# Optimization experiments

Hardware: AMD Instinct MI355X
Metric: run time of the kernel (lower is better)

The kernel has to match this reference:

```python
import jax, jax.numpy as jnp
import numpy as np

D_MODEL = 1024
NUM_HEADS = 16
D_K = D_MODEL // NUM_HEADS  # 64
THETA = 10000.0
B, S = 2, 2048


def _rope(x, cos, sin):
    # x: [b, h, s, d]; cos/sin: [s, d//2] (broadcast over b, h)
    x1 = x[..., 0::2]
    x2 = x[..., 1::2]
    y1 = x1 * cos - x2 * sin
    y2 = x1 * sin + x2 * cos
    # interleave back: stack on last dim then flatten pairs
    return jnp.stack([y1, y2], axis=-1).reshape(x.shape)


def setup_inputs() -> dict:
    key = jax.random.key(0)
    ks = jax.random.split(key, 5)
    scale = 1.0 / np.sqrt(D_MODEL)
    return {
        "x": jax.random.normal(ks[0], (B, S, D_MODEL), dtype=jnp.float32),
        "token_positions": jnp.arange(S, dtype=jnp.int32),
        "Wq": jax.random.normal(ks[1], (D_MODEL, D_MODEL), dtype=jnp.float32) * scale,
        "Wk": jax.random.normal(ks[2], (D_MODEL, D_MODEL), dtype=jnp.float32) * scale,
        "Wv": jax.random.normal(ks[3], (D_MODEL, D_MODEL), dtype=jnp.float32) * scale,
        "Wo": jax.random.normal(ks[4], (D_MODEL, D_MODEL), dtype=jnp.float32) * scale,
    }


def reference(x, token_positions, Wq, Wk, Wv, Wo):
    b, s, _ = x.shape
    # torch nn.Linear semantics (no bias in this repo's Linear): y = x @ W.T
    q = jnp.einsum("bsd,od->bso", x, Wq)
    k = jnp.einsum("bsd,od->bso", x, Wk)
    v = jnp.einsum("bsd,od->bso", x, Wv)
    # split heads: b s (h d) -> b h s d
    def split(t):
        return t.reshape(b, s, NUM_HEADS, D_K).transpose(0, 2, 1, 3)
    q, k, v = split(q), split(k), split(v)

    # RoPE tables
    inv_freq = 1.0 / (THETA ** (jnp.arange(0, D_K, 2, dtype=jnp.float32) / D_K))  # [d/2]
    freqs = token_positions.astype(jnp.float32)[:, None] * inv_freq[None, :]      # [s, d/2]
    cos, sin = jnp.cos(freqs), jnp.sin(freqs)
    q = _rope(q, cos, sin)
    k = _rope(k, cos, sin)

    scale = D_K ** (-0.5)
    scores = jnp.einsum("bhqd,bhkd->bhqk", q, k) * scale  # [b,h,s,s]
    causal = jnp.tril(jnp.ones((s, s), dtype=bool))
    scores = jnp.where(causal, scores, -jnp.inf)
    attn = jax.nn.softmax(scores, axis=-1)
    out = jnp.einsum("bhqk,bhkd->bhqd", attn, v)
    out = out.transpose(0, 2, 1, 3).reshape(b, s, D_MODEL)  # b h s d -> b s (h d)
    return jnp.einsum("bsd,od->bso", out, Wo)
```

## Files before the change

kernel.cpp:

```cpp
#include <hip/hip_runtime.h>
#include <hip/hip_bf16.h>
#include <math.h>

#define SS 2048

typedef __attribute__((ext_vector_type(8))) __bf16 bf16x8;
typedef __attribute__((ext_vector_type(4))) float f32x4;
typedef __attribute__((ext_vector_type(16))) float f32x16;
typedef __attribute__((ext_vector_type(4))) unsigned int u32x4;
typedef __attribute__((ext_vector_type(4))) unsigned short u16x4;

__device__ __forceinline__ f32x4 mfma16(bf16x8 a, bf16x8 b, f32x4 c) {
  return __builtin_amdgcn_mfma_f32_16x16x32_bf16(a, b, c, 0, 0, 0);
}
__device__ __forceinline__ f32x16 mfma32(bf16x8 a, bf16x8 b, f32x16 c) {
  return __builtin_amdgcn_mfma_f32_32x32x16_bf16(a, b, c, 0, 0, 0);
}

__device__ __forceinline__ void gld_lds16(const void* g, void* l) {
  __builtin_amdgcn_global_load_lds(
      (__attribute__((address_space(1))) void*)(g),
      (__attribute__((address_space(3))) void*)(l), 16, 0, 0);
}

#if __has_builtin(__builtin_amdgcn_exp2f)
#define EXP2F(x) __builtin_amdgcn_exp2f(x)
#else
#define EXP2F(x) __expf(0.69314718056f * (x))
#endif

__device__ __forceinline__ unsigned int cvtpk_bf16(float lo, float hi) {
  unsigned int r;
  asm("v_cvt_pk_bf16_f32 %0, %1, %2" : "=v"(r) : "v"(lo), "v"(hi));
  return r;
}
__device__ __forceinline__ void swap32(unsigned int& x, unsigned int& y) {
  asm("v_permlane32_swap_b32 %0, %1" : "+v"(x), "+v"(y));
}
__device__ __forceinline__ unsigned short bfu(float v) {
  __bf16 h = (__bf16)v;
  return __builtin_bit_cast(unsigned short, h);
}

__global__ void prep_kernel(const float* __restrict__ x, const float* __restrict__ Wq,
                            const float* __restrict__ Wk, const float* __restrict__ Wv,
                            const float* __restrict__ Wo, const int* __restrict__ pos,
                            __bf16* __restrict__ xb, __bf16* __restrict__ Wb,
                            float2* __restrict__ tab) {
  const int bid = blockIdx.x, tid = threadIdx.x;
  if (bid >= 4096) {
    int i = (bid - 4096) * 256 + tid;
    int s = i >> 5, j = i & 31;
    float p = (float)pos[s];
    float inv = exp2f((float)j * -0.41524101186098283f);
    float f = p * inv;
    float sn, cs;
    sincosf(f, &sn, &cs);
    tab[i] = make_float2(cs, sn);
    return;
  }
  const float* s;
  __bf16* d;
  size_t base;
  if (bid < 2048) { s = x; d = xb; base = bid; }
  else {
    int seg = (bid - 2048) >> 9;
    s = (seg == 0) ? Wq : (seg == 1) ? Wk : (seg == 2) ? Wv : Wo;
    d = Wb + (size_t)seg * 1024 * 1024;
    base = (bid - 2048) & 511;
  }
  size_t i = (base * 256 + tid) * 8;
  float4 a = *reinterpret_cast<const float4*>(s + i);
  float4 b = *reinterpret_cast<const float4*>(s + i + 4);
  bf16x8 o;
  o[0] = (__bf16)a.x; o[1] = (__bf16)a.y; o[2] = (__bf16)a.z; o[3] = (__bf16)a.w;
  o[4] = (__bf16)b.x; o[5] = (__bf16)b.y; o[6] = (__bf16)b.z; o[7] = (__bf16)b.w;
  *reinterpret_cast<bf16x8*>(d + i) = o;
}

__global__ __launch_bounds__(512, 1) void gemm256_kernel(
    const __bf16* __restrict__ A, const __bf16* __restrict__ Bw,
    __bf16* __restrict__ C, __bf16* __restrict__ Vt,
    const float2* __restrict__ tab) {
  const int K = 1024, N = 3072, nk = 32;
  __shared__ __align__(16) __bf16 sm[57344];
  __bf16* lsA = sm;
  __bf16* lsB = sm + 32768;

  const int tid = threadIdx.x;
  const int lane = tid & 63;
  const int wave = tid >> 6;
  const int wr = wave >> 2, wc = wave & 3;
  const bool lowW = wave < 6;

  const int xcd = blockIdx.x & 7;
  const int ii = blockIdx.x >> 3;
  const int m0 = (2 * xcd + (ii & 1)) * 256;
  const int n0 = (ii >> 1) * 192;

  const f32x4 fzero = {0.f, 0.f, 0.f, 0.f};
  f32x4 acc[8][3];
#pragma unroll
  for (int f = 0; f < 8; ++f)
#pragma unroll
    for (int g = 0; g < 3; ++g) acc[f][g] = fzero;

  const int arow0 = tid >> 2, ac = tid & 3;
  const __bf16* gA0 = A + (size_t)(m0 + arow0) * K + 8 * (ac ^ ((arow0 >> 1) & 3));
  const __bf16* gA1 = A + (size_t)(m0 + 128 + arow0) * K + 8 * (ac ^ (((arow0 + 128) >> 1) & 3));
  const int bid0 = tid, bid1 = tid + 384;
  const int br0 = bid0 >> 2, br1 = bid1 >> 2;
  const __bf16* gB0 = Bw + (size_t)(n0 + br0) * K + 8 * ((bid0 & 3) ^ ((br0 >> 1) & 3));
  const __bf16* gB1 = Bw + (size_t)(n0 + br1) * K + 8 * ((bid1 & 3) ^ ((br1 >> 1) & 3));

#define STAGE256(kt_)                                                \
  do {                                                               \
    const int kc_ = (kt_) & 3;                                       \
    const int ko_ = (kt_) * 32;                                      \
    gld_lds16(gA0 + ko_, lsA + kc_ * 8192 + tid * 8);                \
    gld_lds16(gA1 + ko_, lsA + kc_ * 8192 + 4096 + tid * 8);         \
    if (lowW) {                                                      \
      gld_lds16(gB0 + ko_, lsB + kc_ * 6144 + tid * 8);              \
      gld_lds16(gB1 + ko_, lsB + kc_ * 6144 + 3072 + tid * 8);       \
    }                                                                \
  } while (0)

  STAGE256(0);
  STAGE256(1);

  const int lrow = lane & 15, hi = lane >> 4;

#pragma unroll 1
  for (int kt = 0; kt < nk; ++kt) {
    const int ksA = (kt & 3) * 8192, ksB = (kt & 3) * 6144;
    if (kt + 2 < nk) {
      STAGE256(kt + 2);
      if (lowW) asm volatile("s_waitcnt vmcnt(8)" ::: "memory");
      else      asm volatile("s_waitcnt vmcnt(4)" ::: "memory");
    } else if (kt == nk - 2) {
      if (lowW) asm volatile("s_waitcnt vmcnt(4)" ::: "memory");
      else      asm volatile("s_waitcnt vmcnt(2)" ::: "memory");
    } else {
      asm volatile("s_waitcnt vmcnt(0)" ::: "memory");
    }
    __builtin_amdgcn_s_barrier();

    bf16x8 bfr[3];
#pragma unroll
    for (int g = 0; g < 3; ++g) {
      const int r = wc * 48 + g * 16 + lrow;
      bfr[g] = *reinterpret_cast<const bf16x8*>(
          lsB + ksB + r * 32 + ((hi ^ ((r >> 1) & 3)) * 8));
    }
    bf16x8 af[4];
#pragma unroll
    for (int f = 0; f < 4; ++f) {
      const int r = wr * 128 + f * 16 + lrow;
      af[f] = *reinterpret_cast<const bf16x8*>(
          lsA + ksA + r * 32 + ((hi ^ ((r >> 1) & 3)) * 8));
    }
    __builtin_amdgcn_s_setprio(1);
#pragma unroll
    for (int f = 0; f < 4; ++f)
#pragma unroll
      for (int g = 0; g < 3; ++g) acc[f][g] = mfma16(af[f], bfr[g], acc[f][g]);
    __builtin_amdgcn_s_setprio(0);
#pragma unroll
    for (int f = 0; f < 4; ++f) {
      const int r = wr * 128 + (f + 4) * 16 + lrow;
      af[f] = *reinterpret_cast<const bf16x8*>(
          lsA + ksA + r * 32 + ((hi ^ ((r >> 1) & 3)) * 8));
    }
    __builtin_amdgcn_s_setprio(1);
#pragma unroll
    for (int f = 0; f < 4; ++f)
#pragma unroll
      for (int g = 0; g < 3; ++g) acc[f + 4][g] = mfma16(af[f], bfr[g], acc[f + 4][g]);
    __builtin_amdgcn_s_setprio(0);
  }
#undef STAGE256

  const int crow = (lane >> 4) * 4, ccol = lane & 15;
  const int par = ccol & 1;
#pragma unroll
  for (int g = 0; g < 3; ++g) {
    const int cb = n0 + wc * 48 + g * 16;
    if (cb < 2048) {
      const int jj = ((cb + ccol) >> 1) & 31;
#pragma unroll
      for (int f = 0; f < 8; ++f) {
#pragma unroll
        for (int t = 0; t < 4; ++t) {
          const int r = m0 + wr * 128 + f * 16 + crow + t;
          const int s = r & (SS - 1);
          float2 cs = tab[(s << 5) | jj];
          float v = acc[f][g][t];
          float o = __shfl_xor(v, 1);
          float y = par ? fmaf(o, cs.y, v * cs.x) : fmaf(v, cs.x, -o * cs.y);
          C[(size_t)r * N + cb + ccol] = (__bf16)y;
        }
      }
    } else {
      const int c = cb - 2048 + ccol;
      const int hh = c >> 6, dd = c & 63;
#pragma unroll
      for (int f = 0; f < 8; ++f) {
        const int r0 = m0 + wr * 128 + f * 16 + crow;
        const int bb = r0 >> 11, s0 = r0 & (SS - 1);
        u16x4 pk;
#pragma unroll
        for (int t = 0; t < 4; ++t) pk[t] = bfu(acc[f][g][t]);
        *reinterpret_cast<u16x4*>(Vt + ((size_t)(bb * 16 + hh) * 64 + dd) * SS + s0) = pk;
      }
    }
  }
}

__global__ __launch_bounds__(512, 1) void gemm_out_kernel(
    const __bf16* __restrict__ A, const __bf16* __restrict__ Bw,
    float* __restrict__ C) {
  const int K = 1024, N = 1024, nk = 32;
  __shared__ __align__(16) __bf16 sm[32768];
  __bf16* lsA = sm;
  __bf16* lsB = sm + 16384;

  const int tid = threadIdx.x;
  const int lane = tid & 63;
  const int wave = tid >> 6;
  const int wr = wave >> 2, wc = wave & 3;

  const int xcd = blockIdx.x & 7;
  const int ii = blockIdx.x >> 3;
  const int m0 = (4 * xcd + (ii & 3)) * 128;
  const int n0 = (ii >> 2) * 128;

  const f32x4 fzero = {0.f, 0.f, 0.f, 0.f};
  f32x4 acc[4][2];
#pragma unroll
  for (int f = 0; f < 4; ++f)
#pragma unroll
    for (int g = 0; g < 2; ++g) acc[f][g] = fzero;

  const int srow = tid >> 2, sc = tid & 3;
  const int ssc = 8 * (sc ^ ((srow >> 1) & 3));
  const __bf16* gA = A + (size_t)(m0 + srow) * K + ssc;
  const __bf16* gB = Bw + (size_t)(n0 + srow) * K + ssc;

#define STAGEO(kt_)                                        \
  do {                                                     \
    const int kc_ = (kt_) & 3;                             \
    gld_lds16(gA + (kt_) * 32, lsA + kc_ * 4096 + tid * 8);\
    gld_lds16(gB + (kt_) * 32, lsB + kc_ * 4096 + tid * 8);\
  } while (0)

  STAGEO(0);
  STAGEO(1);

  const int lrow = lane & 15, hi = lane >> 4;

#pragma unroll 1
  for (int kt = 0; kt < nk; ++kt) {
    const int ks = (kt & 3) * 4096;
    if (kt + 2 < nk) {
      STAGEO(kt + 2);
      asm volatile("s_waitcnt vmcnt(4)" ::: "memory");
    } else if (kt == nk - 2) {
      asm volatile("s_waitcnt vmcnt(2)" ::: "memory");
    } else {
      asm volatile("s_waitcnt vmcnt(0)" ::: "memory");
    }
    __builtin_amdgcn_s_barrier();

    bf16x8 bfr[2], af[4];
#pragma unroll
    for (int g = 0; g < 2; ++g) {
      const int r = wc * 32 + g * 16 + lrow;
      bfr[g] = *reinterpret_cast<const bf16x8*>(
          lsB + ks + r * 32 + ((hi ^ ((r >> 1) & 3)) * 8));
    }
#pragma unroll
    for (int f = 0; f < 4; ++f) {
      const int r = wr * 64 + f * 16 + lrow;
      af[f] = *reinterpret_cast<const bf16x8*>(
          lsA + ks + r * 32 + ((hi ^ ((r >> 1) & 3)) * 8));
    }
    __builtin_amdgcn_s_setprio(1);
#pragma unroll
    for (int f = 0; f < 4; ++f)
#pragma unroll
      for (int g = 0; g < 2; ++g) acc[f][g] = mfma16(af[f], bfr[g], acc[f][g]);
    __builtin_amdgcn_s_setprio(0);
  }
#undef STAGEO

  const int crow = (lane >> 4) * 4, ccol = lane & 15;
#pragma unroll
  for (int f = 0; f < 4; ++f) {
#pragma unroll
    for (int g = 0; g < 2; ++g) {
      int r = m0 + wr * 64 + f * 16 + crow;
      int c = n0 + wc * 32 + g * 16 + ccol;
#pragma unroll
      for (int t = 0; t < 4; ++t) C[(size_t)(r + t) * N + c] = acc[f][g][t];
    }
  }
}

#define CEXP 0.18033688011112042f
#define SHIFT_B 16.0f

#define EXPSUM(S0, S1, L)                                                   \
  {                                                                         \
    float a0_ = 0.f, a1_ = 0.f, a2_ = 0.f, a3_ = 0.f;                       \
    _Pragma("unroll") for (int r = 0; r < 16; r += 4) {                     \
      S0[r] = EXP2F(fmaf(S0[r], CEXP, -SHIFT_B)); a0_ += S0[r];             \
      S0[r + 1] = EXP2F(fmaf(S0[r + 1], CEXP, -SHIFT_B)); a1_ += S0[r + 1]; \
      S0[r + 2] = EXP2F(fmaf(S0[r + 2], CEXP, -SHIFT_B)); a2_ += S0[r + 2]; \
      S0[r + 3] = EXP2F(fmaf(S0[r + 3], CEXP, -SHIFT_B)); a3_ += S0[r + 3]; \
    }                                                                       \
    _Pragma("unroll") for (int r = 0; r < 16; r += 4) {                     \
      S1[r] = EXP2F(fmaf(S1[r], CEXP, -SHIFT_B)); a0_ += S1[r];             \
      S1[r + 1] = EXP2F(fmaf(S1[r + 1], CEXP, -SHIFT_B)); a1_ += S1[r + 1]; \
      S1[r + 2] = EXP2F(fmaf(S1[r + 2], CEXP, -SHIFT_B)); a2_ += S1[r + 2]; \
      S1[r + 3] = EXP2F(fmaf(S1[r + 3], CEXP, -SHIFT_B)); a3_ += S1[r + 3]; \
    }                                                                       \
    float rs_ = (a0_ + a1_) + (a2_ + a3_);                                  \
    rs_ += __shfl_xor(rs_, 32);                                             \
    L += rs_;                                                               \
  }

__global__ __launch_bounds__(128) void attn_kernel(const __bf16* __restrict__ qkv,
                                                   const __bf16* __restrict__ Vt,
                                                   __bf16* __restrict__ AO) {
  const int bid = blockIdx.x;
  const int x = bid & 7, t7 = bid >> 3;
  const int low = t7 & 7, phi = (t7 >> 3) & 3, g = t7 >> 5;
  const int p = phi * 8 + x;
  const int b = p >> 4, h = p & 15;
  const int qt = (g == 0) ? low : (g == 1) ? 31 - low : (g == 2) ? 15 - low : 16 + low;

  const int tid = threadIdx.x;
  const int wave = tid >> 6, lane = tid & 63;
  const int q32 = lane & 31, hi = lane >> 5;
  const int qw0 = qt * 64 + wave * 32;
  const int q = qw0 + q32;

  __shared__ __align__(16) __bf16 smem[16384];
  __bf16* lK0 = smem;
  __bf16* lV0 = smem + 8192;

  bf16x8 qb[4];
  {
    const __bf16* qr = qkv + (size_t)(b * SS + q) * 3072 + h * 64;
#pragma unroll
    for (int slot = 0; slot < 4; ++slot)
      qb[slot] = *reinterpret_cast<const bf16x8*>(qr + slot * 16 + hi * 8);
  }
  asm volatile("s_waitcnt vmcnt(0)" ::: "memory");

  const __bf16* kbase = qkv + (size_t)(b * SS) * 3072 + 1024 + h * 64;
  const __bf16* vbase = Vt + (size_t)((b * 16 + h) * 64) * SS;

  const int srow = tid >> 3, scg = tid & 7;
  const int ssc = 8 * (scg ^ (srow & 7));
  const __bf16* kG0 = kbase + (size_t)srow * 3072 + ssc;
  const __bf16* vG0 = vbase + (size_t)srow * SS + ssc;

#define STAGE(buf_, kt_)                                                      \
  do {                                                                        \
    const __bf16* kG = kG0 + (size_t)(kt_)*64 * 3072;                         \
    const __bf16* vG = vG0 + (size_t)(kt_)*64;                                \
    _Pragma("unroll") for (int u = 0; u < 4; ++u) {                           \
      gld_lds16(kG + (size_t)u * 16 * 3072, lK0 + (buf_)*4096 + tid * 8 + u * 1024); \
      gld_lds16(vG + (size_t)u * 16 * SS, lV0 + (buf_)*4096 + tid * 8 + u * 1024);   \
    }                                                                         \
  } while (0)

  f32x16 o0 = {0,0,0,0,0,0,0,0,0,0,0,0,0,0,0,0};
  f32x16 o1 = {0,0,0,0,0,0,0,0,0,0,0,0,0,0,0,0};
  float lsum = 0.f;

  const int nkt = qt + 1;
  STAGE(0, 0);

#pragma unroll 1
  for (int kt = 0; kt < nkt; ++kt) {
    const int buf = kt & 1;
    const int kvb = kt * 64;
    if (kt + 1 < nkt) {
      STAGE(buf ^ 1, kt + 1);
      asm volatile("s_waitcnt vmcnt(8)" ::: "memory");
    } else {
      asm volatile("s_waitcnt vmcnt(0)" ::: "memory");
    }
    __builtin_amdgcn_s_barrier();

    const __bf16* lk = lK0 + buf * 4096;
    const __bf16* lv = lV0 + buf * 4096;

    f32x16 s0 = {0,0,0,0,0,0,0,0,0,0,0,0,0,0,0,0};
    f32x16 s1 = {0,0,0,0,0,0,0,0,0,0,0,0,0,0,0,0};
    __builtin_amdgcn_s_setprio(1);
#pragma unroll
    for (int slot = 0; slot < 4; ++slot) {
      const int swz = 8 * ((slot * 2 + hi) ^ (q32 & 7));
      bf16x8 k0 = *reinterpret_cast<const bf16x8*>(lk + q32 * 64 + swz);
      bf16x8 k1 = *reinterpret_cast<const bf16x8*>(lk + (32 + q32) * 64 + swz);
      s0 = mfma32(k0, qb[slot], s0);
      s1 = mfma32(k1, qb[slot], s1);
    }
    __builtin_amdgcn_s_setprio(0);

    if (kt == qt) {
#pragma unroll
      for (int r = 0; r < 16; ++r) {
        const int rowc = (r & 3) + 8 * (r >> 2) + 4 * hi;
        if (kvb + rowc > q) s0[r] = -INFINITY;
        if (kvb + 32 + rowc > q) s1[r] = -INFINITY;
      }
    }

    EXPSUM(s0, s1, lsum)

    bf16x8 pb[4];
    {
      unsigned int A = cvtpk_bf16(s0[0], s0[1]), B2 = cvtpk_bf16(s0[2], s0[3]);
      unsigned int C2 = cvtpk_bf16(s0[4], s0[5]), D2 = cvtpk_bf16(s0[6], s0[7]);
      swap32(A, C2); swap32(B2, D2);
      u32x4 t0 = {A, B2, C2, D2};
      pb[0] = __builtin_bit_cast(bf16x8, t0);
      unsigned int E = cvtpk_bf16(s0[8], s0[9]), F = cvtpk_bf16(s0[10], s0[11]);
      unsigned int G = cvtpk_bf16(s0[12], s0[13]), H = cvtpk_bf16(s0[14], s0[15]);
      swap32(E, G); swap32(F, H);
      u32x4 t1 = {E, F, G, H};
      pb[1] = __builtin_bit_cast(bf16x8, t1);
      unsigned int A3 = cvtpk_bf16(s1[0], s1[1]), B3 = cvtpk_bf16(s1[2], s1[3]);
      unsigned int C3 = cvtpk_bf16(s1[4], s1[5]), D3 = cvtpk_bf16(s1[6], s1[7]);
      swap32(A3, C3); swap32(B3, D3);
      u32x4 t2 = {A3, B3, C3, D3};
      pb[2] = __builtin_bit_cast(bf16x8, t2);
      unsigned int E3 = cvtpk_bf16(s1[8], s1[9]), F3 = cvtpk_bf16(s1[10], s1[11]);
      unsigned int G3 = cvtpk_bf16(s1[12], s1[13]), H3 = cvtpk_bf16(s1[14], s1[15]);
      swap32(E3, G3); swap32(F3, H3);
      u32x4 t3 = {E3, F3, G3, H3};
      pb[3] = __builtin_bit_cast(bf16x8, t3);
    }

    __builtin_amdgcn_s_setprio(1);
#pragma unroll
    for (int slot = 0; slot < 4; ++slot) {
      const int swz = 8 * ((slot * 2 + hi) ^ (q32 & 7));
      bf16x8 v0 = *reinterpret_cast<const bf16x8*>(lv + q32 * 64 + swz);
      bf16x8 v1 = *reinterpret_cast<const bf16x8*>(lv + (32 + q32) * 64 + swz);
      o0 = mfma32(v0, pb[slot], o0);
      o1 = mfma32(v1, pb[slot], o1);
    }
    __builtin_amdgcn_s_setprio(0);

    __builtin_amdgcn_s_barrier();
  }

  const float inv = 1.0f / lsum;
  __bf16* ol = smem + wave * 2304;
#pragma unroll
  for (int r = 0; r < 16; ++r) {
    const int d = (r & 3) + 8 * (r >> 2) + 4 * hi;
    ol[q32 * 72 + d] = (__bf16)(o0[r] * inv);
    ol[q32 * 72 + 32 + d] = (__bf16)(o1[r] * inv);
  }
#pragma unroll
  for (int pass = 0; pass < 4; ++pass) {
    const int idx = pass * 64 + lane;
    const int row = idx >> 3, colc = idx & 7;
    bf16x8 v = *reinterpret_cast<const bf16x8*>(ol + row * 72 + colc * 8);
    *reinterpret_cast<bf16x8*>(
        AO + (size_t)(b * SS + qt * 64 + wave * 32 + row) * 1024 + h * 64 + colc * 8) = v;
  }
#undef STAGE
}

extern "C" void kernel_launch(void* const* d_in, const int* in_sizes, int n_in,
                              void* d_out, int out_size, void* d_ws, size_t ws_size,
                              hipStream_t stream) {
  const float* x  = (const float*)d_in[0];
  const int* pos  = (const int*)d_in[1];
  const float* Wq = (const float*)d_in[2];
  const float* Wk = (const float*)d_in[3];
  const float* Wv = (const float*)d_in[4];
  const float* Wo = (const float*)d_in[5];

  __bf16* xb  = (__bf16*)d_ws;
  __bf16* Wb  = xb + (size_t)4096 * 1024;
  __bf16* qkv = Wb + (size_t)4096 * 1024;
  __bf16* Vt  = qkv + (size_t)4096 * 3072;
  __bf16* ao  = Vt + (size_t)2048 * 2048;
  float2* tab = (float2*)(ao + (size_t)4096 * 1024);

  prep_kernel<<<4352, 256, 0, stream>>>(x, Wq, Wk, Wv, Wo, pos, xb, Wb, tab);
  gemm256_kernel<<<256, 512, 0, stream>>>(xb, Wb, qkv, Vt, tab);
  attn_kernel<<<1024, 128, 0, stream>>>(qkv, Vt, ao);
  gemm_out_kernel<<<256, 512, 0, stream>>>(ao, Wb + (size_t)3 * 1024 * 1024, (float*)d_out);
}
```

Measured before the change: 103.7 us.

## Software-pipeline attention loop: compute next QK^T before current softmax and PV

Restructures the attention inner loop so that the QK^T MFMAs for tile k+1 are issued before the exp/sum and PV MFMAs of tile k. Score accumulators ping-pong between two register sets. K tiles are double-buffered and V tiles triple-buffered in LDS, with loads staged two tiles ahead. The aim is to overlap the matrix-core work with the softmax VALU work and to hide global-load latency. In exchange it uses more LDS and registers, which may cut occupancy, and the vmcnt wait bookkeeping becomes more complex.

```diff
diff --git a/kernel.cpp b/kernel.cpp
--- a/kernel.cpp
+++ b/kernel.cpp
@@ -329,6 +329,30 @@
     L += rs_;                                                               \
   }
 
+#define CVTPB(S0, S1, PB)                                                   \
+  {                                                                         \
+    unsigned int A_ = cvtpk_bf16(S0[0], S0[1]), B_ = cvtpk_bf16(S0[2], S0[3]); \
+    unsigned int C_ = cvtpk_bf16(S0[4], S0[5]), D_ = cvtpk_bf16(S0[6], S0[7]); \
+    swap32(A_, C_); swap32(B_, D_);                                         \
+    u32x4 t0_ = {A_, B_, C_, D_};                                           \
+    PB[0] = __builtin_bit_cast(bf16x8, t0_);                                \
+    unsigned int E_ = cvtpk_bf16(S0[8], S0[9]), F_ = cvtpk_bf16(S0[10], S0[11]); \
+    unsigned int G_ = cvtpk_bf16(S0[12], S0[13]), H_ = cvtpk_bf16(S0[14], S0[15]); \
+    swap32(E_, G_); swap32(F_, H_);                                         \
+    u32x4 t1_ = {E_, F_, G_, H_};                                           \
+    PB[1] = __builtin_bit_cast(bf16x8, t1_);                                \
+    unsigned int I_ = cvtpk_bf16(S1[0], S1[1]), J_ = cvtpk_bf16(S1[2], S1[3]); \
+    unsigned int K_ = cvtpk_bf16(S1[4], S1[5]), L_ = cvtpk_bf16(S1[6], S1[7]); \
+    swap32(I_, K_); swap32(J_, L_);                                         \
+    u32x4 t2_ = {I_, J_, K_, L_};                                           \
+    PB[2] = __builtin_bit_cast(bf16x8, t2_);                                \
+    unsigned int M_ = cvtpk_bf16(S1[8], S1[9]), N_ = cvtpk_bf16(S1[10], S1[11]); \
+    unsigned int O_ = cvtpk_bf16(S1[12], S1[13]), P_ = cvtpk_bf16(S1[14], S1[15]); \
+    swap32(M_, O_); swap32(N_, P_);                                         \
+    u32x4 t3_ = {M_, N_, O_, P_};                                           \
+    PB[3] = __builtin_bit_cast(bf16x8, t3_);                                \
+  }
+
 __global__ __launch_bounds__(128) void attn_kernel(const __bf16* __restrict__ qkv,
                                                    const __bf16* __restrict__ Vt,
                                                    __bf16* __restrict__ AO) {
@@ -345,7 +369,7 @@
   const int qw0 = qt * 64 + wave * 32;
   const int q = qw0 + q32;
 
-  __shared__ __align__(16) __bf16 smem[16384];
+  __shared__ __align__(16) __bf16 smem[20480];
   __bf16* lK0 = smem;
   __bf16* lV0 = smem + 8192;
 
@@ -366,99 +390,94 @@
   const __bf16* kG0 = kbase + (size_t)srow * 3072 + ssc;
   const __bf16* vG0 = vbase + (size_t)srow * SS + ssc;
 
-#define STAGE(buf_, kt_)                                                      \
+#define STAGE(kt_)                                                            \
   do {                                                                        \
     const __bf16* kG = kG0 + (size_t)(kt_)*64 * 3072;                         \
     const __bf16* vG = vG0 + (size_t)(kt_)*64;                                \
-    _Pragma("unroll") for (int u = 0; u < 4; ++u) {                           \
-      gld_lds16(kG + (size_t)u * 16 * 3072, lK0 + (buf_)*4096 + tid * 8 + u * 1024); \
-      gld_lds16(vG + (size_t)u * 16 * SS, lV0 + (buf_)*4096 + tid * 8 + u * 1024);   \
+    __bf16* lk_ = lK0 + ((kt_)&1) * 4096;                                     \
+    __bf16* lv_ = lV0 + ((kt_)%3) * 4096;                                     \
+    _Pragma("unroll") for (int u = 0; u < 4; ++u)                             \
+      gld_lds16(kG + (size_t)u * 16 * 3072, lk_ + tid * 8 + u * 1024);        \
+    _Pragma("unroll") for (int u = 0; u < 4; ++u)                             \
+      gld_lds16(vG + (size_t)u * 16 * SS, lv_ + tid * 8 + u * 1024);          \
+  } while (0)
+
+#define QKCOMP(ksl_, N0, N1)                                                  \
+  {                                                                           \
+    const __bf16* lk_ = lK0 + (ksl_) * 4096;                                  \
+    __builtin_amdgcn_s_setprio(1);                                            \
+    _Pragma("unroll") for (int slot = 0; slot < 4; ++slot) {                  \
+      const int swz = 8 * ((slot * 2 + hi) ^ (q32 & 7));                      \
+      bf16x8 k0 = *reinterpret_cast<const bf16x8*>(lk_ + q32 * 64 + swz);     \
+      bf16x8 k1 = *reinterpret_cast<const bf16x8*>(lk_ + (32 + q32) * 64 + swz); \
+      N0 = mfma32(k0, qb[slot], N0);                                          \
+      N1 = mfma32(k1, qb[slot], N1);                                          \
     }                                                                         \
-  } while (0)
-
-  f32x16 o0 = {0,0,0,0,0,0,0,0,0,0,0,0,0,0,0,0};
-  f32x16 o1 = {0,0,0,0,0,0,0,0,0,0,0,0,0,0,0,0};
+    __builtin_amdgcn_s_setprio(0);                                            \
+  }
+
+  const f32x16 fz16 = {0,0,0,0,0,0,0,0,0,0,0,0,0,0,0,0};
+  f32x16 o0 = fz16, o1 = fz16;
   float lsum = 0.f;
-
   const int nkt = qt + 1;
-  STAGE(0, 0);
+
+#define ROUND(k_, C0, C1, N0, N1)                                             \
+  {                                                                           \
+    if ((k_) + 2 < nkt) {                                                     \
+      STAGE((k_) + 2);                                                        \
+      asm volatile("s_waitcnt vmcnt(12)" ::: "memory");                       \
+    } else if ((k_) + 1 < nkt) {                                              \
+      asm volatile("s_waitcnt vmcnt(4)" ::: "memory");                        \
+    } else {                                                                  \
+      asm volatile("s_waitcnt vmcnt(0)" ::: "memory");                        \
+    }                                                                         \
+    __builtin_amdgcn_s_barrier();                                             \
+    if ((k_) + 1 < nkt) {                                                     \
+      N0 = fz16; N1 = fz16;                                                   \
+      QKCOMP((((k_) + 1) & 1), N0, N1)                                        \
+    }                                                                         \
+    if ((k_) == nkt - 1) {                    \
+      const int kvb_ = (k_) * 64;                                             \
+      _Pragma("unroll") for (int r = 0; r < 16; ++r) {                        \
+        const int rowc = (r & 3) + 8 * (r >> 2) + 4 * hi;                     \
+        if (kvb_ + rowc > q) C0[r] = -INFINITY;                               \
+        if (kvb_ + 32 + rowc > q) C1[r] = -INFINITY;                          \
+      }                                                                       \
+    }                                                                         \
+    EXPSUM(C0, C1, lsum)                                                      \
+    bf16x8 pb[4];                                                             \
+    CVTPB(C0, C1, pb)                                                         \
+    {                                                                         \
+      const __bf16* lv_ = lV0 + ((k_) % 3) * 4096;                            \
+      __builtin_amdgcn_s_setprio(1);                                          \
+      _Pragma("unroll") for (int slot = 0; slot < 4; ++slot) {                \
+        const int swz = 8 * ((slot * 2 + hi) ^ (q32 & 7));                    \
+        bf16x8 v0 = *reinterpret_cast<const bf16x8*>(lv_ + q32 * 64 + swz);   \
+        bf16x8 v1 = *reinterpret_cast<const bf16x8*>(lv_ + (32 + q32) * 64 + swz); \
+        o0 = mfma32(v0, pb[slot], o0);                                        \
+        o1 = mfma32(v1, pb[slot], o1);                                        \
+      }                                                                       \
+      __builtin_amdgcn_s_setprio(0);                                          \
+    }                                                                         \
+    __builtin_amdgcn_s_barrier();                                             \
+  }
+
+  STAGE(0);
+  STAGE(1);
+  asm volatile("s_waitcnt vmcnt(12)" ::: "memory");
+  __builtin_amdgcn_s_barrier();
+  f32x16 sE0 = fz16, sE1 = fz16, sO0 = fz16, sO1 = fz16;
+  QKCOMP(0, sE0, sE1)
+  __builtin_amdgcn_s_barrier();
 
 #pragma unroll 1
-  for (int kt = 0; kt < nkt; ++kt) {
-    const int buf = kt & 1;
-    const int kvb = kt * 64;
-    if (kt + 1 < nkt) {
-      STAGE(buf ^ 1, kt + 1);
-      asm volatile("s_waitcnt vmcnt(8)" ::: "memory");
-    } else {
-      asm volatile("s_waitcnt vmcnt(0)" ::: "memory");
-    }
-    __builtin_amdgcn_s_barrier();
-
-    const __bf16* lk = lK0 + buf * 4096;
-    const __bf16* lv = lV0 + buf * 4096;
-
-    f32x16 s0 = {0,0,0,0,0,0,0,0,0,0,0,0,0,0,0,0};
-    f32x16 s1 = {0,0,0,0,0,0,0,0,0,0,0,0,0,0,0,0};
-    __builtin_amdgcn_s_setprio(1);
-#pragma unroll
-    for (int slot = 0; slot < 4; ++slot) {
-      const int swz = 8 * ((slot * 2 + hi) ^ (q32 & 7));
-      bf16x8 k0 = *reinterpret_cast<const bf16x8*>(lk + q32 * 64 + swz);
-      bf16x8 k1 = *reinterpret_cast<const bf16x8*>(lk + (32 + q32) * 64 + swz);
-      s0 = mfma32(k0, qb[slot], s0);
-      s1 = mfma32(k1, qb[slot], s1);
-    }
-    __builtin_amdgcn_s_setprio(0);
-
-    if (kt == qt) {
-#pragma unroll
-      for (int r = 0; r < 16; ++r) {
-        const int rowc = (r & 3) + 8 * (r >> 2) + 4 * hi;
-        if (kvb + rowc > q) s0[r] = -INFINITY;
-        if (kvb + 32 + rowc > q) s1[r] = -INFINITY;
-      }
-    }
-
-    EXPSUM(s0, s1, lsum)
-
-    bf16x8 pb[4];
-    {
-      unsigned int A = cvtpk_bf16(s0[0], s0[1]), B2 = cvtpk_bf16(s0[2], s0[3]);
-      unsigned int C2 = cvtpk_bf16(s0[4], s0[5]), D2 = cvtpk_bf16(s0[6], s0[7]);
-      swap32(A, C2); swap32(B2, D2);
-      u32x4 t0 = {A, B2, C2, D2};
-      pb[0] = __builtin_bit_cast(bf16x8, t0);
-      unsigned int E = cvtpk_bf16(s0[8], s0[9]), F = cvtpk_bf16(s0[10], s0[11]);
-      unsigned int G = cvtpk_bf16(s0[12], s0[13]), H = cvtpk_bf16(s0[14], s0[15]);
-      swap32(E, G); swap32(F, H);
-      u32x4 t1 = {E, F, G, H};
-      pb[1] = __builtin_bit_cast(bf16x8, t1);
-      unsigned int A3 = cvtpk_bf16(s1[0], s1[1]), B3 = cvtpk_bf16(s1[2], s1[3]);
-      unsigned int C3 = cvtpk_bf16(s1[4], s1[5]), D3 = cvtpk_bf16(s1[6], s1[7]);
-      swap32(A3, C3); swap32(B3, D3);
-      u32x4 t2 = {A3, B3, C3, D3};
-      pb[2] = __builtin_bit_cast(bf16x8, t2);
-      unsigned int E3 = cvtpk_bf16(s1[8], s1[9]), F3 = cvtpk_bf16(s1[10], s1[11]);
-      unsigned int G3 = cvtpk_bf16(s1[12], s1[13]), H3 = cvtpk_bf16(s1[14], s1[15]);
-      swap32(E3, G3); swap32(F3, H3);
-      u32x4 t3 = {E3, F3, G3, H3};
-      pb[3] = __builtin_bit_cast(bf16x8, t3);
-    }
-
-    __builtin_amdgcn_s_setprio(1);
-#pragma unroll
-    for (int slot = 0; slot < 4; ++slot) {
-      const int swz = 8 * ((slot * 2 + hi) ^ (q32 & 7));
-      bf16x8 v0 = *reinterpret_cast<const bf16x8*>(lv + q32 * 64 + swz);
-      bf16x8 v1 = *reinterpret_cast<const bf16x8*>(lv + (32 + q32) * 64 + swz);
-      o0 = mfma32(v0, pb[slot], o0);
-      o1 = mfma32(v1, pb[slot], o1);
-    }
-    __builtin_amdgcn_s_setprio(0);
-
-    __builtin_amdgcn_s_barrier();
-  }
+  for (int kk = 0; kk < nkt; kk += 2) {
+    ROUND(kk, sE0, sE1, sO0, sO1)
+    if (kk + 1 < nkt) ROUND(kk + 1, sO0, sO1, sE0, sE1)
+  }
+#undef ROUND
+#undef QKCOMP
+#undef STAGE
 
   const float inv = 1.0f / lsum;
   __bf16* ol = smem + wave * 2304;
@@ -476,7 +495,6 @@
     *reinterpret_cast<bf16x8*>(
         AO + (size_t)(b * SS + qt * 64 + wave * 32 + row) * 1024 + h * 64 + colc * 8) = v;
   }
-#undef STAGE
 }
 
 extern "C" void kernel_launch(void* const* d_in, const int* in_sizes, int n_in,
```

Result: slower. 119.6 us (+15.4%).

## Split causal attention KV range across two blocks and add combine kernel

Applied to the files above, without the earlier changes.

Each query tile's KV loop is split into two halves handled by separate blocks, doubling the grid. Each half writes unnormalized partial outputs and row sums, and a new combine kernel adds the two and normalizes. This is meant to shorten the long tail of late query tiles and raise parallelism. In exchange it drops the double-buffered K/V prefetch for a single buffer with a full wait every iteration, and adds an extra kernel launch plus a round trip of partial outputs through memory. Rounding the unnormalized partials to bf16 may also cost some accuracy.

```diff
diff --git a/kernel.cpp b/kernel.cpp
--- a/kernel.cpp
+++ b/kernel.cpp
@@ -329,15 +329,24 @@
     L += rs_;                                                               \
   }
 
+template <int SPLIT>
 __global__ __launch_bounds__(128) void attn_kernel(const __bf16* __restrict__ qkv,
                                                    const __bf16* __restrict__ Vt,
-                                                   __bf16* __restrict__ AO) {
+                                                   __bf16* __restrict__ pA,
+                                                   __bf16* __restrict__ pB,
+                                                   float* __restrict__ pL) {
   const int bid = blockIdx.x;
-  const int x = bid & 7, t7 = bid >> 3;
-  const int low = t7 & 7, phi = (t7 >> 3) & 3, g = t7 >> 5;
-  const int p = phi * 8 + x;
-  const int b = p >> 4, h = p & 15;
+  const int x = bid & 7, t8 = bid >> 3;
+  const int low = t8 & 7, phi = (t8 >> 3) & 3, g = (t8 >> 5) & 3;
+  const int half = SPLIT ? (t8 >> 7) : 0;
+  const int hp = phi * 8 + x;
+  const int b = hp >> 4, h = hp & 15;
   const int qt = (g == 0) ? low : (g == 1) ? 31 - low : (g == 2) ? 15 - low : 16 + low;
+
+  const int nkt = qt + 1;
+  const int mid = (nkt + 1) >> 1;
+  const int k0 = SPLIT ? (half ? mid : 0) : 0;
+  const int k1 = SPLIT ? (half ? nkt : mid) : nkt;
 
   const int tid = threadIdx.x;
   const int wave = tid >> 6, lane = tid & 63;
@@ -345,9 +354,7 @@
   const int qw0 = qt * 64 + wave * 32;
   const int q = qw0 + q32;
 
-  __shared__ __align__(16) __bf16 smem[16384];
-  __bf16* lK0 = smem;
-  __bf16* lV0 = smem + 8192;
+  __shared__ __align__(16) __bf16 smem[8192];
 
   bf16x8 qb[4];
   {
@@ -356,7 +363,6 @@
     for (int slot = 0; slot < 4; ++slot)
       qb[slot] = *reinterpret_cast<const bf16x8*>(qr + slot * 16 + hi * 8);
   }
-  asm volatile("s_waitcnt vmcnt(0)" ::: "memory");
 
   const __bf16* kbase = qkv + (size_t)(b * SS) * 3072 + 1024 + h * 64;
   const __bf16* vbase = Vt + (size_t)((b * 16 + h) * 64) * SS;
@@ -366,52 +372,39 @@
   const __bf16* kG0 = kbase + (size_t)srow * 3072 + ssc;
   const __bf16* vG0 = vbase + (size_t)srow * SS + ssc;
 
-#define STAGE(buf_, kt_)                                                      \
-  do {                                                                        \
-    const __bf16* kG = kG0 + (size_t)(kt_)*64 * 3072;                         \
-    const __bf16* vG = vG0 + (size_t)(kt_)*64;                                \
-    _Pragma("unroll") for (int u = 0; u < 4; ++u) {                           \
-      gld_lds16(kG + (size_t)u * 16 * 3072, lK0 + (buf_)*4096 + tid * 8 + u * 1024); \
-      gld_lds16(vG + (size_t)u * 16 * SS, lV0 + (buf_)*4096 + tid * 8 + u * 1024);   \
-    }                                                                         \
-  } while (0)
-
-  f32x16 o0 = {0,0,0,0,0,0,0,0,0,0,0,0,0,0,0,0};
-  f32x16 o1 = {0,0,0,0,0,0,0,0,0,0,0,0,0,0,0,0};
+  const f32x16 fz16 = {0,0,0,0,0,0,0,0,0,0,0,0,0,0,0,0};
+  f32x16 o0 = fz16, o1 = fz16;
   float lsum = 0.f;
 
-  const int nkt = qt + 1;
-  STAGE(0, 0);
-
 #pragma unroll 1
-  for (int kt = 0; kt < nkt; ++kt) {
-    const int buf = kt & 1;
-    const int kvb = kt * 64;
-    if (kt + 1 < nkt) {
-      STAGE(buf ^ 1, kt + 1);
-      asm volatile("s_waitcnt vmcnt(8)" ::: "memory");
-    } else {
-      asm volatile("s_waitcnt vmcnt(0)" ::: "memory");
-    }
+  for (int kt = k0; kt < k1; ++kt) {
+    {
+      const __bf16* kG = kG0 + (size_t)kt * 64 * 3072;
+      const __bf16* vG = vG0 + (size_t)kt * 64;
+#pragma unroll
+      for (int u = 0; u < 4; ++u)
+        gld_lds16(kG + (size_t)u * 16 * 3072, smem + tid * 8 + u * 1024);
+#pragma unroll
+      for (int u = 0; u < 4; ++u)
+        gld_lds16(vG + (size_t)u * 16 * SS, smem + 4096 + tid * 8 + u * 1024);
+    }
+    asm volatile("s_waitcnt vmcnt(0)" ::: "memory");
     __builtin_amdgcn_s_barrier();
 
-    const __bf16* lk = lK0 + buf * 4096;
-    const __bf16* lv = lV0 + buf * 4096;
-
-    f32x16 s0 = {0,0,0,0,0,0,0,0,0,0,0,0,0,0,0,0};
-    f32x16 s1 = {0,0,0,0,0,0,0,0,0,0,0,0,0,0,0,0};
+    f32x16 s0 = fz16, s1 = fz16;
     __builtin_amdgcn_s_setprio(1);
 #pragma unroll
     for (int slot = 0; slot < 4; ++slot) {
       const int swz = 8 * ((slot * 2 + hi) ^ (q32 & 7));
-      bf16x8 k0 = *reinterpret_cast<const bf16x8*>(lk + q32 * 64 + swz);
-      bf16x8 k1 = *reinterpret_cast<const bf16x8*>(lk + (32 + q32) * 64 + swz);
-      s0 = mfma32(k0, qb[slot], s0);
-      s1 = mfma32(k1, qb[slot], s1);
+      bf16x8 kf0 = *reinterpret_cast<const bf16x8*>(smem + q32 * 64 + swz);
+      bf16x8 kf1 = *reinterpret_cast<const bf16x8*>(smem + (32 + q32) * 64 + swz);
+      s0 = mfma32(kf0, qb[slot], s0);
+      s1 = mfma32(kf1, qb[slot], s1);
     }
     __builtin_amdgcn_s_setprio(0);
 
     if (kt == qt) {
+      const int kvb = kt * 64;
 #pragma unroll
       for (int r = 0; r < 16; ++r) {
         const int rowc = (r & 3) + 8 * (r >> 2) + 4 * hi;
@@ -450,8 +443,8 @@
 #pragma unroll
     for (int slot = 0; slot < 4; ++slot) {
       const int swz = 8 * ((slot * 2 + hi) ^ (q32 & 7));
-      bf16x8 v0 = *reinterpret_cast<const bf16x8*>(lv + q32 * 64 + swz);
-      bf16x8 v1 = *reinterpret_cast<const bf16x8*>(lv + (32 + q32) * 64 + swz);
+      bf16x8 v0 = *reinterpret_cast<const bf16x8*>(smem + 4096 + q32 * 64 + swz);
+      bf16x8 v1 = *reinterpret_cast<const bf16x8*>(smem + 4096 + (32 + q32) * 64 + swz);
       o0 = mfma32(v0, pb[slot], o0);
       o1 = mfma32(v1, pb[slot], o1);
     }
@@ -460,23 +453,48 @@
     __builtin_amdgcn_s_barrier();
   }
 
-  const float inv = 1.0f / lsum;
+  const float inv = SPLIT ? 1.0f : (1.0f / lsum);
   __bf16* ol = smem + wave * 2304;
 #pragma unroll
   for (int r = 0; r < 16; ++r) {
     const int d = (r & 3) + 8 * (r >> 2) + 4 * hi;
-    ol[q32 * 72 + d] = (__bf16)(o0[r] * inv);
-    ol[q32 * 72 + 32 + d] = (__bf16)(o1[r] * inv);
-  }
+    if (SPLIT) {
+      ol[q32 * 72 + d] = (__bf16)o0[r];
+      ol[q32 * 72 + 32 + d] = (__bf16)o1[r];
+    } else {
+      ol[q32 * 72 + d] = (__bf16)(o0[r] * inv);
+      ol[q32 * 72 + 32 + d] = (__bf16)(o1[r] * inv);
+    }
+  }
+  __bf16* dst = (SPLIT && half) ? pB : pA;
 #pragma unroll
   for (int pass = 0; pass < 4; ++pass) {
     const int idx = pass * 64 + lane;
     const int row = idx >> 3, colc = idx & 7;
     bf16x8 v = *reinterpret_cast<const bf16x8*>(ol + row * 72 + colc * 8);
     *reinterpret_cast<bf16x8*>(
-        AO + (size_t)(b * SS + qt * 64 + wave * 32 + row) * 1024 + h * 64 + colc * 8) = v;
-  }
-#undef STAGE
+        dst + (size_t)(b * SS + qt * 64 + wave * 32 + row) * 1024 + h * 64 + colc * 8) = v;
+  }
+  if (SPLIT && hi == 0)
+    pL[half * 65536 + hp * 2048 + qt * 64 + wave * 32 + q32] = lsum;
+}
+
+__global__ void combine_kernel(const __bf16* __restrict__ pB,
+                               const float* __restrict__ pL,
+                               __bf16* __restrict__ ao) {
+  const int i = (blockIdx.x * 256 + threadIdx.x) * 8;
+  const int row = i >> 10, col = i & 1023;
+  const int bb = row >> 11, s = row & 2047, h = col >> 6;
+  const int bh = bb * 16 + h;
+  const float lA = pL[bh * 2048 + s];
+  const float lB = pL[65536 + bh * 2048 + s];
+  const float inv = 1.0f / (lA + lB);
+  bf16x8 a = *reinterpret_cast<const bf16x8*>(ao + i);
+  bf16x8 b8 = *reinterpret_cast<const bf16x8*>(pB + i);
+  bf16x8 o;
+#pragma unroll
+  for (int j = 0; j < 8; ++j) o[j] = (__bf16)(((float)a[j] + (float)b8[j]) * inv);
+  *reinterpret_cast<bf16x8*>(ao + i) = o;
 }
 
 extern "C" void kernel_launch(void* const* d_in, const int* in_sizes, int n_in,
@@ -495,9 +513,18 @@
   __bf16* Vt  = qkv + (size_t)4096 * 3072;
   __bf16* ao  = Vt + (size_t)2048 * 2048;
   float2* tab = (float2*)(ao + (size_t)4096 * 1024);
+  __bf16* pB  = (__bf16*)(tab + 2048 * 32);
+  float*  pL  = (float*)(pB + (size_t)4096 * 1024);
+
+  const size_t NEED = (size_t)(pL + 2 * 32 * 2048) - (size_t)d_ws;
 
   prep_kernel<<<4352, 256, 0, stream>>>(x, Wq, Wk, Wv, Wo, pos, xb, Wb, tab);
   gemm256_kernel<<<256, 512, 0, stream>>>(xb, Wb, qkv, Vt, tab);
-  attn_kernel<<<1024, 128, 0, stream>>>(qkv, Vt, ao);
+  if (ws_size >= NEED) {
+    attn_kernel<1><<<2048, 128, 0, stream>>>(qkv, Vt, ao, pB, pL);
+    combine_kernel<<<2048, 256, 0, stream>>>(pB, pL, ao);
+  } else {
+    attn_kernel<0><<<1024, 128, 0, stream>>>(qkv, Vt, ao, nullptr, nullptr);
+  }
   gemm_out_kernel<<<256, 512, 0, stream>>>(ao, Wb + (size_t)3 * 1024 * 1024, (float*)d_out);
 }
```

After: 104.7 us. No clear change (+1.0%).
